# Kernel optimization log

Measured on AMD Instinct MI355X. Metric: run time of the kernel, lower is better.

## Reference

```python
import jax, jax.numpy as jnp
import numpy as np

MARGIN = 1.0
B, D_FEAT = 4096, 256


def setup_inputs() -> dict:
    key = jax.random.key(0)
    return {"inputs": jax.random.normal(key, (B, D_FEAT), dtype=jnp.float32)}


def reference(inputs):
    bsz = inputs.shape[0]
    P = bsz // 2  # number of positive pairs
    # pairwise similarity, scaled as in the original (/128.0)
    D = jnp.matmul(inputs, inputs.T) / 128.0          # [B, B]
    Dexpm = jnp.exp(MARGIN + D)                        # [B, B]

    # Row 2p over odd columns (2k+1), row 2p+1 over even columns (2l)
    Rodd = Dexpm[0::2, 1::2]                           # [P, P]: Dexpm[2p, 2k+1]
    Reven = Dexpm[1::2, 0::2]                          # [P, P]: Dexpm[2p+1, 2l]

    p = jnp.arange(P)
    k = jnp.arange(P)
    # Faithful to the original code's exclusion bug: k != pos_j (=2p+1), l != pos_i (=2p)
    mask_i = (k[None, :] != (2 * p + 1)[:, None]).astype(Dexpm.dtype)  # [P, P]
    mask_j = (k[None, :] != (2 * p)[:, None]).astype(Dexpm.dtype)      # [P, P]

    neg_ik = jnp.sum(Rodd * mask_i, axis=1)            # [P]
    neg_jl = jnp.sum(Reven * mask_j, axis=1)           # [P]

    Dpos = D[2 * p, 2 * p + 1]                         # [P] positive-pair similarity
    J = jnp.log(1e-8 + neg_ik + neg_jl) - Dpos         # [P]
    return jnp.sum(jnp.maximum(J, 0.0) ** 2) / bsz
```

## Files before the change

### kernel.cpp

```cpp
#include <hip/hip_runtime.h>

#define PN 2048

typedef __attribute__((ext_vector_type(8))) short short8;
typedef __attribute__((ext_vector_type(4))) float f32x4;

static __device__ __forceinline__ unsigned int pk_bf2(float lo, float hi) {
    unsigned int ul = __float_as_uint(lo);
    unsigned int uh = __float_as_uint(hi);
    ul = (ul + 0x7fffu + ((ul >> 16) & 1u)) >> 16;
    uh = (uh + 0x7fffu + ((uh >> 16) & 1u)) >> 16;
    return ul | (uh << 16);
}


__global__ __launch_bounds__(256, 2) void sml_mfma(
    const float* __restrict__ X, float* __restrict__ Srow, float* __restrict__ Scol,
    float* __restrict__ Dpos, float* __restrict__ Ex1, float* __restrict__ Ex2,
    float* __restrict__ out)
{
    __shared__ __align__(16) unsigned int A_s[128 * 32];
    __shared__ __align__(16) unsigned int B_s[64 * 32];
    __shared__ float red[2][128];
    __shared__ float red2[2][64];

    const int bx = blockIdx.x, by = blockIdx.y;
    const int t = threadIdx.x;
    const int lane = t & 63, wid = t >> 6;
    const int wr = wid >> 1, wc = wid & 1;
    const int g4 = lane >> 4, rl = lane & 15;

    if (bx == 0 && by == 0 && t == 0) out[0] = 0.f;

    const int s  = t & 7;
    const int r0 = t >> 3;

    const float* aptr[4];
    const float* bptr[2];
    #pragma unroll
    for (int q = 0; q < 4; ++q)
        aptr[q] = X + (size_t)(2 * (bx * 128 + r0 + 32 * q)) * 256 + s * 8;
    #pragma unroll
    for (int q = 0; q < 2; ++q)
        bptr[q] = X + (size_t)(2 * (by * 64 + r0 + 32 * q) + 1) * 256 + s * 8;

    f32x4 acc[4][2];
    #pragma unroll
    for (int i = 0; i < 4; ++i)
        #pragma unroll
        for (int j = 0; j < 2; ++j) acc[i][j] = (f32x4){0.f, 0.f, 0.f, 0.f};

    float4 pa[4][2], pb[2][2];
    #pragma unroll
    for (int q = 0; q < 4; ++q) {
        pa[q][0] = *(const float4*)(aptr[q]);
        pa[q][1] = *(const float4*)(aptr[q] + 4);
    }
    #pragma unroll
    for (int q = 0; q < 2; ++q) {
        pb[q][0] = *(const float4*)(bptr[q]);
        pb[q][1] = *(const float4*)(bptr[q] + 4);
    }

    for (int ks = 0; ks < 4; ++ks) {
        __syncthreads();
        #pragma unroll
        for (int q = 0; q < 4; ++q) {
            const int r  = r0 + 32 * q;
            const int sw = (s ^ (r & 7)) << 2;
            uint4 wa = { pk_bf2(pa[q][0].x, pa[q][0].y), pk_bf2(pa[q][0].z, pa[q][0].w),
                         pk_bf2(pa[q][1].x, pa[q][1].y), pk_bf2(pa[q][1].z, pa[q][1].w) };
            *(uint4*)&A_s[r * 32 + sw] = wa;
        }
        #pragma unroll
        for (int q = 0; q < 2; ++q) {
            const int r  = r0 + 32 * q;
            const int sw = (s ^ (r & 7)) << 2;
            uint4 wb = { pk_bf2(pb[q][0].x, pb[q][0].y), pk_bf2(pb[q][0].z, pb[q][0].w),
                         pk_bf2(pb[q][1].x, pb[q][1].y), pk_bf2(pb[q][1].z, pb[q][1].w) };
            *(uint4*)&B_s[r * 32 + sw] = wb;
        }
        __syncthreads();
        if (ks < 3) {
            const int off = (ks + 1) * 64;
            #pragma unroll
            for (int q = 0; q < 4; ++q) {
                pa[q][0] = *(const float4*)(aptr[q] + off);
                pa[q][1] = *(const float4*)(aptr[q] + off + 4);
            }
            #pragma unroll
            for (int q = 0; q < 2; ++q) {
                pb[q][0] = *(const float4*)(bptr[q] + off);
                pb[q][1] = *(const float4*)(bptr[q] + off + 4);
            }
        }
        #pragma unroll
        for (int kk = 0; kk < 2; ++kk) {
            short8 af[4], bfj[2];
            #pragma unroll
            for (int i = 0; i < 4; ++i) {
                const int r  = wr * 64 + i * 16 + rl;
                const int sl = (kk * 4 + g4) ^ (r & 7);
                af[i] = *(const short8*)&A_s[r * 32 + sl * 4];
            }
            #pragma unroll
            for (int j = 0; j < 2; ++j) {
                const int r  = wc * 32 + j * 16 + rl;
                const int sl = (kk * 4 + g4) ^ (r & 7);
                bfj[j] = *(const short8*)&B_s[r * 32 + sl * 4];
            }
            #pragma unroll
            for (int i = 0; i < 4; ++i)
                #pragma unroll
                for (int j = 0; j < 2; ++j)
                    acc[i][j] = __builtin_amdgcn_mfma_f32_16x16x32_bf16(af[i], bfj[j], acc[i][j], 0, 0, 0);
        }
    }

    float rs[4][4];
    float cs[2] = {0.f, 0.f};
    #pragma unroll
    for (int i = 0; i < 4; ++i)
        #pragma unroll
        for (int rg = 0; rg < 4; ++rg) rs[i][rg] = 0.f;

    #pragma unroll
    for (int i = 0; i < 4; ++i) {
        #pragma unroll
        for (int j = 0; j < 2; ++j) {
            const int kg = by * 64 + wc * 32 + j * 16 + rl;
            #pragma unroll
            for (int rg = 0; rg < 4; ++rg) {
                const int pg = bx * 128 + wr * 64 + i * 16 + g4 * 4 + rg;
                const float c = acc[i][j][rg] * (1.f / 128.f);
                const float e = __expf(1.f + c);
                if (kg == pg) Dpos[pg] = c;
                if (kg == 2 * pg + 1) Ex1[pg] = e;
                if (pg == 2 * kg) Ex2[kg] = e;
                rs[i][rg] += e;
                cs[j] += e;
            }
        }
    }

    #pragma unroll
    for (int i = 0; i < 4; ++i) {
        #pragma unroll
        for (int rg = 0; rg < 4; ++rg) {
            float v = rs[i][rg];
            v += __shfl_xor(v, 1); v += __shfl_xor(v, 2);
            v += __shfl_xor(v, 4); v += __shfl_xor(v, 8);
            if (rl == 0) red[wc][wr * 64 + i * 16 + g4 * 4 + rg] = v;
        }
    }
    #pragma unroll
    for (int j = 0; j < 2; ++j) {
        float v = cs[j];
        v += __shfl_xor(v, 16); v += __shfl_xor(v, 32);
        if (g4 == 0) red2[wr][wc * 32 + j * 16 + rl] = v;
    }
    __syncthreads();
    if (t < 128)
        Srow[by * PN + bx * 128 + t] = red[0][t] + red[1][t];
    else if (t < 192)
        Scol[bx * PN + by * 64 + (t - 128)] = red2[0][t - 128] + red2[1][t - 128];
}

__global__ __launch_bounds__(64) void sml_finish(
    const float* __restrict__ Srow, const float* __restrict__ Scol,
    const float* __restrict__ Dpos, const float* __restrict__ Ex1,
    const float* __restrict__ Ex2, float* __restrict__ out)
{
    const int t = threadIdx.x;
    const int p = blockIdx.x * 64 + t;
    float ssum = 0.f;
    #pragma unroll
    for (int g = 0; g < 32; ++g) ssum += Srow[g * PN + p];
    #pragma unroll
    for (int g = 0; g < 16; ++g) ssum += Scol[g * PN + p];
    if (p < 1024) ssum -= Ex1[p] + Ex2[p];
    const float J = __logf(1e-8f + ssum) - Dpos[p];
    const float v = fmaxf(J, 0.f);
    float local = v * v;
    #pragma unroll
    for (int m = 1; m < 64; m <<= 1) local += __shfl_xor(local, m);
    if (t == 0) atomicAdd(out, local * (1.f / 4096.f));
}

extern "C" void kernel_launch(void* const* d_in, const int* in_sizes, int n_in,
                              void* d_out, int out_size, void* d_ws, size_t ws_size,
                              hipStream_t stream) {
    const float* X = (const float*)d_in[0];
    float* ws   = (float*)d_ws;
    float* Srow = ws;
    float* Scol = Srow + 32 * PN;
    float* Dpos = Scol + 16 * PN;
    float* Ex1  = Dpos + PN;
    float* Ex2  = Ex1 + PN;
    float* out  = (float*)d_out;

    dim3 g1(16, 32);
    sml_mfma<<<g1, dim3(256), 0, stream>>>(X, Srow, Scol, Dpos, Ex1, Ex2, out);
    sml_finish<<<32, dim3(64), 0, stream>>>(Srow, Scol, Dpos, Ex1, Ex2, out);
}
```

Baseline: 19.60 us.

## Fuse finish pass into MFMA kernel via atomics and last-block reduction

Removes the separate finish kernel. Each block now atomically adds its row and column exp-sums into a single Neg array, with the excluded terms masked out in registers instead of being stored and subtracted later. A global counter picks the last block, which computes the log/hinge/square reduction and writes the output. This saves a kernel launch and the partial-sum round trip, but adds a memset, float atomic contention on 2048 addresses, and order-dependent float summation.

```diff
diff --git a/kernel.cpp b/kernel.cpp
--- a/kernel.cpp
+++ b/kernel.cpp
@@ -14,23 +14,21 @@
 }
 
 
-__global__ __launch_bounds__(256, 2) void sml_mfma(
-    const float* __restrict__ X, float* __restrict__ Srow, float* __restrict__ Scol,
-    float* __restrict__ Dpos, float* __restrict__ Ex1, float* __restrict__ Ex2,
-    float* __restrict__ out)
+__global__ __launch_bounds__(256, 2) void sml_fused(
+    const float* __restrict__ X, float* __restrict__ Neg, unsigned int* __restrict__ cnt,
+    float* __restrict__ Dpos, float* __restrict__ out)
 {
     __shared__ __align__(16) unsigned int A_s[128 * 32];
     __shared__ __align__(16) unsigned int B_s[64 * 32];
     __shared__ float red[2][128];
     __shared__ float red2[2][64];
+    __shared__ unsigned int lastflag;
 
     const int bx = blockIdx.x, by = blockIdx.y;
     const int t = threadIdx.x;
     const int lane = t & 63, wid = t >> 6;
     const int wr = wid >> 1, wc = wid & 1;
     const int g4 = lane >> 4, rl = lane & 15;
-
-    if (bx == 0 && by == 0 && t == 0) out[0] = 0.f;
 
     const int s  = t & 7;
     const int r0 = t >> 3;
@@ -134,11 +132,10 @@
                 const int pg = bx * 128 + wr * 64 + i * 16 + g4 * 4 + rg;
                 const float c = acc[i][j][rg] * (1.f / 128.f);
                 const float e = __expf(1.f + c);
-                if (kg == pg) Dpos[pg] = c;
-                if (kg == 2 * pg + 1) Ex1[pg] = e;
-                if (pg == 2 * kg) Ex2[kg] = e;
-                rs[i][rg] += e;
-                cs[j] += e;
+                if (kg == pg)
+                    __hip_atomic_store(&Dpos[pg], c, __ATOMIC_RELAXED, __HIP_MEMORY_SCOPE_AGENT);
+                rs[i][rg] += (kg == 2 * pg + 1) ? 0.f : e;
+                cs[j]     += (pg == 2 * kg)     ? 0.f : e;
             }
         }
     }
@@ -161,30 +158,36 @@
     }
     __syncthreads();
     if (t < 128)
-        Srow[by * PN + bx * 128 + t] = red[0][t] + red[1][t];
+        atomicAdd(&Neg[bx * 128 + t], red[0][t] + red[1][t]);
     else if (t < 192)
-        Scol[bx * PN + by * 64 + (t - 128)] = red2[0][t - 128] + red2[1][t - 128];
-}
-
-__global__ __launch_bounds__(64) void sml_finish(
-    const float* __restrict__ Srow, const float* __restrict__ Scol,
-    const float* __restrict__ Dpos, const float* __restrict__ Ex1,
-    const float* __restrict__ Ex2, float* __restrict__ out)
-{
-    const int t = threadIdx.x;
-    const int p = blockIdx.x * 64 + t;
-    float ssum = 0.f;
-    #pragma unroll
-    for (int g = 0; g < 32; ++g) ssum += Srow[g * PN + p];
-    #pragma unroll
-    for (int g = 0; g < 16; ++g) ssum += Scol[g * PN + p];
-    if (p < 1024) ssum -= Ex1[p] + Ex2[p];
-    const float J = __logf(1e-8f + ssum) - Dpos[p];
-    const float v = fmaxf(J, 0.f);
-    float local = v * v;
-    #pragma unroll
-    for (int m = 1; m < 64; m <<= 1) local += __shfl_xor(local, m);
-    if (t == 0) atomicAdd(out, local * (1.f / 4096.f));
+        atomicAdd(&Neg[by * 64 + (t - 128)], red2[0][t - 128] + red2[1][t - 128]);
+
+    __syncthreads();
+    if (t == 0) {
+        __threadfence();
+        unsigned int old = __hip_atomic_fetch_add(cnt, 1u, __ATOMIC_ACQ_REL, __HIP_MEMORY_SCOPE_AGENT);
+        lastflag = (old == 511u) ? 1u : 0u;
+    }
+    __syncthreads();
+    if (lastflag) {
+        __threadfence();
+        float local = 0.f;
+        #pragma unroll
+        for (int i = 0; i < 8; ++i) {
+            const int p = t + 256 * i;
+            const float neg = Neg[p];
+            const float dp  = Dpos[p];
+            const float J = __logf(1e-8f + neg) - dp;
+            const float v = fmaxf(J, 0.f);
+            local += v * v;
+        }
+        #pragma unroll
+        for (int m = 1; m < 64; m <<= 1) local += __shfl_xor(local, m);
+        if (lane == 0) red[0][wid] = local;
+        __syncthreads();
+        if (t == 0)
+            out[0] = (red[0][0] + red[0][1] + red[0][2] + red[0][3]) * (1.f / 4096.f);
+    }
 }
 
 extern "C" void kernel_launch(void* const* d_in, const int* in_sizes, int n_in,
@@ -192,14 +195,12 @@
                               hipStream_t stream) {
     const float* X = (const float*)d_in[0];
     float* ws   = (float*)d_ws;
-    float* Srow = ws;
-    float* Scol = Srow + 32 * PN;
-    float* Dpos = Scol + 16 * PN;
-    float* Ex1  = Dpos + PN;
-    float* Ex2  = Ex1 + PN;
+    float* Neg  = ws;
+    unsigned int* cnt = (unsigned int*)(ws + PN);
+    float* Dpos = ws + PN + 256;
     float* out  = (float*)d_out;
 
+    hipMemsetAsync(d_ws, 0, (PN + 1) * sizeof(float), stream);
     dim3 g1(16, 32);
-    sml_mfma<<<g1, dim3(256), 0, stream>>>(X, Srow, Scol, Dpos, Ex1, Ex2, out);
-    sml_finish<<<32, dim3(64), 0, stream>>>(Srow, Scol, Dpos, Ex1, Ex2, out);
+    sml_fused<<<g1, dim3(256), 0, stream>>>(X, Neg, cnt, Dpos, out);
 }
```

New measurement: 36.51 us. 86.3% more time.

## Use 128x128 tiles with 512 threads, two-stage K buffering, inline exclusion masks

Applied to the files above, without the earlier changes.

Grows the column tile from 64 to 128 and uses 8 waves per block, so the grid shrinks to 16x16 blocks and each A tile is reused across twice as many columns. K is now split into two 128-wide chunks held in double-buffered shared memory, with the second chunk's global loads issued before the first chunk's MFMAs. The exclusion of masked entries now happens inside the row and column sums, which removes the Ex1/Ex2 workspace and its subtraction in the finish kernel. The trade-offs are fewer blocks (256) spread over many CUs, much larger shared memory per block, and higher register pressure from holding both prefetch buffers.

```diff
diff --git a/kernel.cpp b/kernel.cpp
--- a/kernel.cpp
+++ b/kernel.cpp
@@ -14,35 +14,33 @@
 }
 
 
-__global__ __launch_bounds__(256, 2) void sml_mfma(
+__global__ __launch_bounds__(512, 2) void sml_mfma(
     const float* __restrict__ X, float* __restrict__ Srow, float* __restrict__ Scol,
-    float* __restrict__ Dpos, float* __restrict__ Ex1, float* __restrict__ Ex2,
-    float* __restrict__ out)
+    float* __restrict__ Dpos, float* __restrict__ out)
 {
-    __shared__ __align__(16) unsigned int A_s[128 * 32];
-    __shared__ __align__(16) unsigned int B_s[64 * 32];
-    __shared__ float red[2][128];
-    __shared__ float red2[2][64];
+    __shared__ __align__(16) unsigned int A_s[2 * 128 * 64];
+    __shared__ __align__(16) unsigned int B_s[2 * 128 * 64];
+    __shared__ float red[4][128];
 
     const int bx = blockIdx.x, by = blockIdx.y;
     const int t = threadIdx.x;
     const int lane = t & 63, wid = t >> 6;
-    const int wr = wid >> 1, wc = wid & 1;
+    const int wr = wid >> 2, wc = wid & 3;
     const int g4 = lane >> 4, rl = lane & 15;
 
     if (bx == 0 && by == 0 && t == 0) out[0] = 0.f;
 
-    const int s  = t & 7;
-    const int r0 = t >> 3;
-
-    const float* aptr[4];
-    const float* bptr[2];
-    #pragma unroll
-    for (int q = 0; q < 4; ++q)
-        aptr[q] = X + (size_t)(2 * (bx * 128 + r0 + 32 * q)) * 256 + s * 8;
-    #pragma unroll
-    for (int q = 0; q < 2; ++q)
-        bptr[q] = X + (size_t)(2 * (by * 64 + r0 + 32 * q) + 1) * 256 + s * 8;
+    const int s  = t & 15;
+    const int r0 = t >> 4;
+
+    const float* aP[4];
+    const float* bP[4];
+    #pragma unroll
+    for (int q = 0; q < 4; ++q) {
+        const int r = r0 + 32 * q;
+        aP[q] = X + (size_t)(2 * (bx * 128 + r)) * 256 + s * 8;
+        bP[q] = X + (size_t)(2 * (by * 128 + r) + 1) * 256 + s * 8;
+    }
 
     f32x4 acc[4][2];
     #pragma unroll
@@ -50,71 +48,87 @@
         #pragma unroll
         for (int j = 0; j < 2; ++j) acc[i][j] = (f32x4){0.f, 0.f, 0.f, 0.f};
 
-    float4 pa[4][2], pb[2][2];
-    #pragma unroll
-    for (int q = 0; q < 4; ++q) {
-        pa[q][0] = *(const float4*)(aptr[q]);
-        pa[q][1] = *(const float4*)(aptr[q] + 4);
-    }
-    #pragma unroll
-    for (int q = 0; q < 2; ++q) {
-        pb[q][0] = *(const float4*)(bptr[q]);
-        pb[q][1] = *(const float4*)(bptr[q] + 4);
-    }
-
-    for (int ks = 0; ks < 4; ++ks) {
-        __syncthreads();
-        #pragma unroll
-        for (int q = 0; q < 4; ++q) {
-            const int r  = r0 + 32 * q;
-            const int sw = (s ^ (r & 7)) << 2;
-            uint4 wa = { pk_bf2(pa[q][0].x, pa[q][0].y), pk_bf2(pa[q][0].z, pa[q][0].w),
-                         pk_bf2(pa[q][1].x, pa[q][1].y), pk_bf2(pa[q][1].z, pa[q][1].w) };
-            *(uint4*)&A_s[r * 32 + sw] = wa;
-        }
-        #pragma unroll
-        for (int q = 0; q < 2; ++q) {
-            const int r  = r0 + 32 * q;
-            const int sw = (s ^ (r & 7)) << 2;
-            uint4 wb = { pk_bf2(pb[q][0].x, pb[q][0].y), pk_bf2(pb[q][0].z, pb[q][0].w),
-                         pk_bf2(pb[q][1].x, pb[q][1].y), pk_bf2(pb[q][1].z, pb[q][1].w) };
-            *(uint4*)&B_s[r * 32 + sw] = wb;
-        }
-        __syncthreads();
-        if (ks < 3) {
-            const int off = (ks + 1) * 64;
+    float4 a0[4][2], b0[4][2];
+    #pragma unroll
+    for (int q = 0; q < 4; ++q) {
+        a0[q][0] = *(const float4*)(aP[q]);     a0[q][1] = *(const float4*)(aP[q] + 4);
+        b0[q][0] = *(const float4*)(bP[q]);     b0[q][1] = *(const float4*)(bP[q] + 4);
+    }
+    #pragma unroll
+    for (int q = 0; q < 4; ++q) {
+        const int r  = r0 + 32 * q;
+        const int sw = (s ^ (r & 15)) << 2;
+        uint4 wa = { pk_bf2(a0[q][0].x, a0[q][0].y), pk_bf2(a0[q][0].z, a0[q][0].w),
+                     pk_bf2(a0[q][1].x, a0[q][1].y), pk_bf2(a0[q][1].z, a0[q][1].w) };
+        uint4 wb = { pk_bf2(b0[q][0].x, b0[q][0].y), pk_bf2(b0[q][0].z, b0[q][0].w),
+                     pk_bf2(b0[q][1].x, b0[q][1].y), pk_bf2(b0[q][1].z, b0[q][1].w) };
+        *(uint4*)&A_s[r * 64 + sw] = wa;
+        *(uint4*)&B_s[r * 64 + sw] = wb;
+    }
+    __syncthreads();
+
+    float4 a1[4][2], b1[4][2];
+    #pragma unroll
+    for (int q = 0; q < 4; ++q) {
+        a1[q][0] = *(const float4*)(aP[q] + 128); a1[q][1] = *(const float4*)(aP[q] + 132);
+        b1[q][0] = *(const float4*)(bP[q] + 128); b1[q][1] = *(const float4*)(bP[q] + 132);
+    }
+
+    #pragma unroll
+    for (int kk = 0; kk < 4; ++kk) {
+        short8 af[4], bfj[2];
+        #pragma unroll
+        for (int i = 0; i < 4; ++i) {
+            const int r  = wr * 64 + i * 16 + rl;
+            const int sl = ((kk << 2) + g4) ^ (r & 15);
+            af[i] = *(const short8*)&A_s[r * 64 + sl * 4];
+        }
+        #pragma unroll
+        for (int j = 0; j < 2; ++j) {
+            const int r  = wc * 32 + j * 16 + rl;
+            const int sl = ((kk << 2) + g4) ^ (r & 15);
+            bfj[j] = *(const short8*)&B_s[r * 64 + sl * 4];
+        }
+        #pragma unroll
+        for (int i = 0; i < 4; ++i)
             #pragma unroll
-            for (int q = 0; q < 4; ++q) {
-                pa[q][0] = *(const float4*)(aptr[q] + off);
-                pa[q][1] = *(const float4*)(aptr[q] + off + 4);
-            }
+            for (int j = 0; j < 2; ++j)
+                acc[i][j] = __builtin_amdgcn_mfma_f32_16x16x32_bf16(af[i], bfj[j], acc[i][j], 0, 0, 0);
+    }
+
+    #pragma unroll
+    for (int q = 0; q < 4; ++q) {
+        const int r  = r0 + 32 * q;
+        const int sw = (s ^ (r & 15)) << 2;
+        uint4 wa = { pk_bf2(a1[q][0].x, a1[q][0].y), pk_bf2(a1[q][0].z, a1[q][0].w),
+                     pk_bf2(a1[q][1].x, a1[q][1].y), pk_bf2(a1[q][1].z, a1[q][1].w) };
+        uint4 wb = { pk_bf2(b1[q][0].x, b1[q][0].y), pk_bf2(b1[q][0].z, b1[q][0].w),
+                     pk_bf2(b1[q][1].x, b1[q][1].y), pk_bf2(b1[q][1].z, b1[q][1].w) };
+        *(uint4*)&A_s[8192 + r * 64 + sw] = wa;
+        *(uint4*)&B_s[8192 + r * 64 + sw] = wb;
+    }
+    __syncthreads();
+
+    #pragma unroll
+    for (int kk = 0; kk < 4; ++kk) {
+        short8 af[4], bfj[2];
+        #pragma unroll
+        for (int i = 0; i < 4; ++i) {
+            const int r  = wr * 64 + i * 16 + rl;
+            const int sl = ((kk << 2) + g4) ^ (r & 15);
+            af[i] = *(const short8*)&A_s[8192 + r * 64 + sl * 4];
+        }
+        #pragma unroll
+        for (int j = 0; j < 2; ++j) {
+            const int r  = wc * 32 + j * 16 + rl;
+            const int sl = ((kk << 2) + g4) ^ (r & 15);
+            bfj[j] = *(const short8*)&B_s[8192 + r * 64 + sl * 4];
+        }
+        #pragma unroll
+        for (int i = 0; i < 4; ++i)
             #pragma unroll
-            for (int q = 0; q < 2; ++q) {
-                pb[q][0] = *(const float4*)(bptr[q] + off);
-                pb[q][1] = *(const float4*)(bptr[q] + off + 4);
-            }
-        }
-        #pragma unroll
-        for (int kk = 0; kk < 2; ++kk) {
-            short8 af[4], bfj[2];
-            #pragma unroll
-            for (int i = 0; i < 4; ++i) {
-                const int r  = wr * 64 + i * 16 + rl;
-                const int sl = (kk * 4 + g4) ^ (r & 7);
-                af[i] = *(const short8*)&A_s[r * 32 + sl * 4];
-            }
-            #pragma unroll
-            for (int j = 0; j < 2; ++j) {
-                const int r  = wc * 32 + j * 16 + rl;
-                const int sl = (kk * 4 + g4) ^ (r & 7);
-                bfj[j] = *(const short8*)&B_s[r * 32 + sl * 4];
-            }
-            #pragma unroll
-            for (int i = 0; i < 4; ++i)
-                #pragma unroll
-                for (int j = 0; j < 2; ++j)
-                    acc[i][j] = __builtin_amdgcn_mfma_f32_16x16x32_bf16(af[i], bfj[j], acc[i][j], 0, 0, 0);
-        }
+            for (int j = 0; j < 2; ++j)
+                acc[i][j] = __builtin_amdgcn_mfma_f32_16x16x32_bf16(af[i], bfj[j], acc[i][j], 0, 0, 0);
     }
 
     float rs[4][4];
@@ -128,17 +142,15 @@
     for (int i = 0; i < 4; ++i) {
         #pragma unroll
         for (int j = 0; j < 2; ++j) {
-            const int kg = by * 64 + wc * 32 + j * 16 + rl;
+            const int kg = by * 128 + wc * 32 + j * 16 + rl;
             #pragma unroll
             for (int rg = 0; rg < 4; ++rg) {
                 const int pg = bx * 128 + wr * 64 + i * 16 + g4 * 4 + rg;
                 const float c = acc[i][j][rg] * (1.f / 128.f);
                 const float e = __expf(1.f + c);
                 if (kg == pg) Dpos[pg] = c;
-                if (kg == 2 * pg + 1) Ex1[pg] = e;
-                if (pg == 2 * kg) Ex2[kg] = e;
-                rs[i][rg] += e;
-                cs[j] += e;
+                rs[i][rg] += (kg == 2 * pg + 1) ? 0.f : e;
+                cs[j]     += (pg == 2 * kg)     ? 0.f : e;
             }
         }
     }
@@ -153,32 +165,33 @@
             if (rl == 0) red[wc][wr * 64 + i * 16 + g4 * 4 + rg] = v;
         }
     }
+    __syncthreads();
+    if (t < 128)
+        Srow[by * PN + bx * 128 + t] = red[0][t] + red[1][t] + red[2][t] + red[3][t];
+    __syncthreads();
+
     #pragma unroll
     for (int j = 0; j < 2; ++j) {
         float v = cs[j];
         v += __shfl_xor(v, 16); v += __shfl_xor(v, 32);
-        if (g4 == 0) red2[wr][wc * 32 + j * 16 + rl] = v;
+        if (g4 == 0) red[wr][wc * 32 + j * 16 + rl] = v;
     }
     __syncthreads();
     if (t < 128)
-        Srow[by * PN + bx * 128 + t] = red[0][t] + red[1][t];
-    else if (t < 192)
-        Scol[bx * PN + by * 64 + (t - 128)] = red2[0][t - 128] + red2[1][t - 128];
+        Scol[bx * PN + by * 128 + t] = red[0][t] + red[1][t];
 }
 
 __global__ __launch_bounds__(64) void sml_finish(
     const float* __restrict__ Srow, const float* __restrict__ Scol,
-    const float* __restrict__ Dpos, const float* __restrict__ Ex1,
-    const float* __restrict__ Ex2, float* __restrict__ out)
+    const float* __restrict__ Dpos, float* __restrict__ out)
 {
     const int t = threadIdx.x;
     const int p = blockIdx.x * 64 + t;
     float ssum = 0.f;
     #pragma unroll
-    for (int g = 0; g < 32; ++g) ssum += Srow[g * PN + p];
+    for (int g = 0; g < 16; ++g) ssum += Srow[g * PN + p];
     #pragma unroll
     for (int g = 0; g < 16; ++g) ssum += Scol[g * PN + p];
-    if (p < 1024) ssum -= Ex1[p] + Ex2[p];
     const float J = __logf(1e-8f + ssum) - Dpos[p];
     const float v = fmaxf(J, 0.f);
     float local = v * v;
@@ -193,13 +206,10 @@
     const float* X = (const float*)d_in[0];
     float* ws   = (float*)d_ws;
     float* Srow = ws;
-    float* Scol = Srow + 32 * PN;
+    float* Scol = Srow + 16 * PN;
     float* Dpos = Scol + 16 * PN;
-    float* Ex1  = Dpos + PN;
-    float* Ex2  = Ex1 + PN;
     float* out  = (float*)d_out;
 
-    dim3 g1(16, 32);
-    sml_mfma<<<g1, dim3(256), 0, stream>>>(X, Srow, Scol, Dpos, Ex1, Ex2, out);
-    sml_finish<<<32, dim3(64), 0, stream>>>(Srow, Scol, Dpos, Ex1, Ex2, out);
-}
+    sml_mfma<<<dim3(16, 16), dim3(512), 0, stream>>>(X, Srow, Scol, Dpos, out);
+    sml_finish<<<32, dim3(64), 0, stream>>>(Srow, Scol, Dpos, out);
+}
```

Result: faster. 16.37 us, median of 2 (-16.5%).
